# Kernel tuning notes

Measured on AMD Instinct MI355X. Metric: run time of the kernel, lower is better.

The kernel has to match this reference:

```python
import jax, jax.numpy as jnp
import numpy as np

VOCAB = 50000
EMB = 512
HID = 1024
B = 256
W = 26


def setup_inputs() -> dict:
    key = jax.random.key(0)
    k0, k1, k2, k3, k4, k5, k6 = jax.random.split(key, 7)
    s = 1.0 / np.sqrt(HID)
    return {
        "ques_vec": jax.random.randint(k0, (B, W), 0, VOCAB + 1, dtype=jnp.int32),
        "ques_len": jax.random.randint(k1, (B,), 1, W + 1, dtype=jnp.int32),
        # nn.Linear(vocab, emb, bias=False).weight -> [emb, vocab]
        "W_emb": jax.random.normal(k2, (EMB, VOCAB), dtype=jnp.float32) * 0.02,
        # PyTorch LSTM params, gate order (i, f, g, o)
        "W_ih": jax.random.uniform(k3, (4 * HID, EMB), jnp.float32, -s, s),
        "W_hh": jax.random.uniform(k4, (4 * HID, HID), jnp.float32, -s, s),
        "b_ih": jax.random.uniform(k5, (4 * HID,), jnp.float32, -s, s),
        "b_hh": jax.random.uniform(k6, (4 * HID,), jnp.float32, -s, s),
    }


def reference(ques_vec, ques_len, W_emb, W_ih, W_hh, b_ih, b_hh):
    # one_hot(vocab+1)[:, :, 1:] @ W_emb.T  ==  gather of W_emb columns;
    # token 0 (pad) maps to the zero embedding.
    tok = ques_vec  # [B, W]
    emb = jnp.where(
        (tok > 0)[..., None],
        W_emb.T[jnp.maximum(tok - 1, 0)],  # [B, W, EMB]
        jnp.zeros((), dtype=W_emb.dtype),
    )
    emb = jnp.tanh(emb)  # tanh(0)=0 for pads, matches torch

    bias = b_ih + b_hh

    def step(carry, xt):
        h, c = carry
        gates = xt @ W_ih.T + h @ W_hh.T + bias  # [B, 4H]
        i, f, g, o = jnp.split(gates, 4, axis=-1)
        c = jax.nn.sigmoid(f) * c + jax.nn.sigmoid(i) * jnp.tanh(g)
        h = jax.nn.sigmoid(o) * jnpp_tanh(c) if False else jax.nn.sigmoid(o) * jnp.tanh(c)
        return (h, c), None

    h0 = jnp.zeros((tok.shape[0], HID), dtype=W_emb.dtype)
    (h_n, _), _ = jax.lax.scan(step, (h0, h0), jnp.swapaxes(emb, 0, 1))
    return h_n  # [B, HID] == h_n.view(B, -1) for 1-layer unidirectional LSTM
```

## Files before the change

### kernel.cpp

```cpp
#include <hip/hip_runtime.h>
#include <hip/hip_bf16.h>

#define VOCAB 50000
#define EMBD  512
#define HID   1024
#define NB    256
#define SEQW  26
#define MTOT  (SEQW * NB)
#define NGATE (4 * HID)

typedef short short8 __attribute__((ext_vector_type(8)));
typedef _Float16 half8 __attribute__((ext_vector_type(8)));
typedef _Float16 half2v __attribute__((ext_vector_type(2)));
typedef float f32x4  __attribute__((ext_vector_type(4)));
typedef float f32x2  __attribute__((ext_vector_type(2)));

__device__ __forceinline__ unsigned short f16bits(_Float16 h) {
    union { _Float16 h; unsigned short u; } cv; cv.h = h; return cv.u;
}

__device__ __forceinline__ void gload16(const void* g, void* l) {
    __builtin_amdgcn_global_load_lds(
        (const __attribute__((address_space(1))) void*)g,
        (__attribute__((address_space(3))) void*)l, 16, 0, 0);
}

__global__ void init_kernel(unsigned short* __restrict__ hBuf,
                            unsigned int* __restrict__ bar) {
    int idx = blockIdx.x * blockDim.x + threadIdx.x;
    hBuf[idx] = 0;
    if (idx < 4096) bar[idx] = 0;
}

__global__ void transp_kernel(const float* __restrict__ W,
                              unsigned short* __restrict__ WT) {
    __shared__ _Float16 tile[64][72];
    int v0 = blockIdx.x * 64;
    int e0 = blockIdx.y * 64;
    int tid = threadIdx.x;

    int e_loc = tid >> 2, q = tid & 3;
    int vq = q * 16;
    if (v0 + vq < VOCAB) {
        const float* src = W + (size_t)(e0 + e_loc) * VOCAB + v0 + vq;
        #pragma unroll
        for (int j = 0; j < 4; ++j) {
            f32x4 x = *(const f32x4*)(src + 4 * j);
            #pragma unroll
            for (int i = 0; i < 4; ++i)
                tile[vq + 4 * j + i][e_loc] = (_Float16)x[i];
        }
    }
    __syncthreads();

    int v_loc = tid >> 2;
    int ec = q * 16;
    int v = v0 + v_loc;
    if (v < VOCAB) {
        short8* dst = (short8*)(WT + (size_t)v * EMBD + e0 + ec);
        dst[0] = *(const short8*)&tile[v_loc][ec];
        dst[1] = *(const short8*)&tile[v_loc][ec + 8];
    }
}

__global__ void embed_kernel(const int* __restrict__ qv,
                             const unsigned short* __restrict__ WT,
                             unsigned short* __restrict__ eHi) {
    int pair = blockIdx.x * 4 + (threadIdx.x >> 6);
    int t = pair >> 8, b = pair & 255;
    int lane = threadIdx.x & 63;
    int tok = qv[b * SEQW + t];
    short8 out = {};
    if (tok > 0) {
        short8 v = *(const short8*)(WT + (size_t)(tok - 1) * EMBD + lane * 8);
        #pragma unroll
        for (int i = 0; i < 8; ++i) {
            union { short s; _Float16 h; } cv; cv.s = v[i];
            out[i] = (short)f16bits((_Float16)tanhf((float)cv.h));
        }
    }
    *(short8*)(eHi + (size_t)pair * EMBD + lane * 8) = out;
}

__global__ void convw_kernel(const float* __restrict__ Wih,
                             const float* __restrict__ Whh,
                             const float* __restrict__ b_ih,
                             const float* __restrict__ b_hh,
                             unsigned short* __restrict__ ih,
                             unsigned short* __restrict__ hh,
                             float* __restrict__ bsum) {
    int j = blockIdx.x;
    if (threadIdx.x == 0) bsum[j] = b_ih[j] + b_hh[j];
    for (int col = threadIdx.x; col < EMBD; col += blockDim.x)
        ih[(size_t)j * EMBD + col] = f16bits((_Float16)Wih[(size_t)j * EMBD + col]);
    for (int col = threadIdx.x; col < HID; col += blockDim.x)
        hh[(size_t)j * HID + col] = f16bits((_Float16)Whh[(size_t)j * HID + col]);
}

__global__ __launch_bounds__(512, 2) void pregemm_kernel(
    const unsigned short* __restrict__ eHi,
    const unsigned short* __restrict__ ih,
    const float* __restrict__ bsum,
    unsigned short* __restrict__ G0h)
{
    __shared__ char smem[65536];

    int id = blockIdx.x;
    int xcd = id & 7, lid = id >> 3;
    int pc = xcd * 4 + (lid & 3);
    int pm = lid >> 2;
    int m0 = pm * 128;

    int tid = threadIdx.x;
    int w = tid >> 6;
    int mh = w >> 2, nh = w & 3;
    int lane = tid & 63;
    int col16 = lane & 15, g4 = lane >> 4;

    int sr = lane >> 3, sc = lane & 7;
    int ra0 = w * 16 + sr, ra1 = ra0 + 8;
    const char* eB = (const char*)eHi;
    const char* iB = (const char*)ih;
    size_t aOffG0 = (size_t)(m0 + ra0) * 1024 + (size_t)(((sc ^ (ra0 & 7))) * 16);
    size_t aOffG1 = (size_t)(m0 + ra1) * 1024 + (size_t)(((sc ^ (ra1 & 7))) * 16);
    int gb0 = (ra0 >> 5) * 1024 + pc * 32 + (ra0 & 31);
    int gb1 = (ra1 >> 5) * 1024 + pc * 32 + (ra1 & 31);
    size_t bOffG0 = (size_t)gb0 * 1024 + (size_t)(((sc ^ (ra0 & 7))) * 16);
    size_t bOffG1 = (size_t)gb1 * 1024 + (size_t)(((sc ^ (ra1 & 7))) * 16);
    int ldsRow0 = (w * 16) * 128;
    int ldsRow1 = (w * 16 + 8) * 128;

    f32x4 acc[4][2];
    #pragma unroll
    for (int fm = 0; fm < 4; ++fm)
        #pragma unroll
        for (int fn = 0; fn < 2; ++fn)
            acc[fm][fn] = (f32x4){0.f, 0.f, 0.f, 0.f};

    int swb = col16 & 7;
    int aRow[4], bRow[2];
    #pragma unroll
    for (int fm = 0; fm < 4; ++fm) aRow[fm] = (mh * 64 + fm * 16 + col16) * 128;
    #pragma unroll
    for (int fn = 0; fn < 2; ++fn) bRow[fn] = (nh * 32 + fn * 16 + col16) * 128;

#define STAGE(kb, buf) do { \
        int kby = (kb) * 128; \
        char* aD = smem + (buf) * 16384; \
        char* bD = smem + 32768 + (buf) * 16384; \
        gload16(eB + aOffG0 + kby, aD + ldsRow0); \
        gload16(eB + aOffG1 + kby, aD + ldsRow1); \
        gload16(iB + bOffG0 + kby, bD + ldsRow0); \
        gload16(iB + bOffG1 + kby, bD + ldsRow1); \
    } while (0)

    STAGE(0, 0);
    #pragma unroll
    for (int kb = 0; kb < 8; ++kb) {
        int cur = kb & 1;
        __syncthreads();
        if (kb < 7) STAGE(kb + 1, cur ^ 1);
        const char* aS = smem + cur * 16384;
        const char* bS = smem + 32768 + cur * 16384;
        #pragma unroll
        for (int kk = 0; kk < 2; ++kk) {
            int co = ((kk * 4 + g4) ^ swb) * 16;
            half8 bF[2];
            #pragma unroll
            for (int fn = 0; fn < 2; ++fn)
                bF[fn] = *(const half8*)(const void*)(bS + bRow[fn] + co);
            #pragma unroll
            for (int fm = 0; fm < 4; ++fm) {
                half8 aF = *(const half8*)(const void*)(aS + aRow[fm] + co);
                #pragma unroll
                for (int fn = 0; fn < 2; ++fn)
                    acc[fm][fn] = __builtin_amdgcn_mfma_f32_16x16x32_f16(
                        aF, bF[fn], acc[fm][fn], 0, 0, 0);
            }
        }
    }
#undef STAGE

    #pragma unroll
    for (int fn = 0; fn < 2; ++fn) {
        int cp = nh * 32 + fn * 16 + col16;
        int gate = cp >> 5;
        int jh = pc * 32 + (cp & 31);
        int ct = jh >> 4, jl = jh & 15;
        int cidx = gate * 16 + jl;
        float bv = bsum[gate * HID + jh];
        #pragma unroll
        for (int fm = 0; fm < 4; ++fm)
            #pragma unroll
            for (int r = 0; r < 4; ++r) {
                int row = m0 + mh * 64 + fm * 16 + g4 * 4 + r;
                int t = row >> 8, b = row & 255;
                G0h[(((size_t)t * 64 + ct) * 256 + b) * 64 + cidx] =
                    f16bits((_Float16)(acc[fm][fn][r] + bv));
            }
    }
}

__global__ __launch_bounds__(512, 2) void lstm_persist(
    const unsigned short* __restrict__ hh,
    unsigned short* __restrict__ hBuf,
    const unsigned short* __restrict__ G0h,
    float* __restrict__ out,
    unsigned int* __restrict__ bar)
{
    extern __shared__ char smem[];
    float* gbuf = (float*)(smem + 65536);

    int bx = blockIdx.x;
    int grp = bx & 7;
    int lid = bx >> 3;
    int m0  = grp * 32;
    int jh0 = lid * 32;

    int tid = threadIdx.x;
    int w = tid >> 6;
    int kq = w >> 2, gate = w & 3;
    int lane = tid & 63;
    int col16 = lane & 15, g4 = lane >> 4;

    unsigned int* flags = bar + grp * 512;

    half8 bB[2][16];
    #pragma unroll
    for (int nf = 0; nf < 2; ++nf) {
        const char* bRow = (const char*)hh +
            (((size_t)(gate * HID + jh0 + nf * 16 + col16)) * HID + kq * 512 + g4 * 8) * 2;
        #pragma unroll
        for (int kk = 0; kk < 16; ++kk)
            bB[nf][kk] = *(const half8*)(const void*)(bRow + kk * 64);
    }

    int srow = tid >> 4, sc = tid & 15;
    int swz = (srow & 7) << 4;
    int swr = (col16 & 7) << 4;
    int ml = srow, jl2 = sc * 2;
    int jh = jh0 + jl2;
    int ctE = jh >> 4, jlE = jh & 15;

    float cReg[2] = {0.f, 0.f};

    for (int t = 0; t < SEQW; ++t) {
        const unsigned short* hIn = hBuf + (size_t)t * NB * HID;
        unsigned short* hOut = hBuf + (size_t)(t + 1) * NB * HID;

        f32x2 g0v[4];
        {
            const unsigned short* pg = G0h +
                (((size_t)t * 64 + ctE) * 256 + (m0 + ml)) * 64 + jlE;
            #pragma unroll
            for (int q = 0; q < 4; ++q) {
                half2v hv = *(const half2v*)(const void*)(pg + q * 16);
                g0v[q] = (f32x2){(float)hv[0], (float)hv[1]};
            }
        }

        f32x4 acc[2][2];
        #pragma unroll
        for (int mf = 0; mf < 2; ++mf)
            #pragma unroll
            for (int nf = 0; nf < 2; ++nf)
                acc[mf][nf] = (f32x4){0.f, 0.f, 0.f, 0.f};

        if (t > 0) {
            {
                const char* hRowB = (const char*)hIn + (size_t)(m0 + srow) * (HID * 2);
                short8 v[8];
                #pragma unroll
                for (int j = 0; j < 8; ++j)
                    v[j] = *(const short8*)(const void*)(hRowB + j * 256 + sc * 16);
                #pragma unroll
                for (int j = 0; j < 8; ++j)
                    *(short8*)(smem + srow * 2048 + ((j * 256 + sc * 16) ^ swz)) = v[j];
            }
            __syncthreads();

            #pragma unroll
            for (int kk = 0; kk < 16; ++kk) {
                int kb = kq * 1024 + kk * 64 + g4 * 16;
                half8 a0 = *(const half8*)(const void*)(smem + col16 * 2048 + (kb ^ swr));
                half8 a1 = *(const half8*)(const void*)(smem + (col16 + 16) * 2048 + (kb ^ swr));
                acc[0][0] = __builtin_amdgcn_mfma_f32_16x16x32_f16(a0, bB[0][kk], acc[0][0], 0, 0, 0);
                acc[0][1] = __builtin_amdgcn_mfma_f32_16x16x32_f16(a0, bB[1][kk], acc[0][1], 0, 0, 0);
                acc[1][0] = __builtin_amdgcn_mfma_f32_16x16x32_f16(a1, bB[0][kk], acc[1][0], 0, 0, 0);
                acc[1][1] = __builtin_amdgcn_mfma_f32_16x16x32_f16(a1, bB[1][kk], acc[1][1], 0, 0, 0);
            }
        }

        #pragma unroll
        for (int mf = 0; mf < 2; ++mf)
            #pragma unroll
            for (int nf = 0; nf < 2; ++nf)
                #pragma unroll
                for (int r = 0; r < 4; ++r)
                    gbuf[(((kq * 4 + gate) * 32) + mf * 16 + g4 * 4 + r) * 36
                         + nf * 16 + col16] = acc[mf][nf][r];
        __syncthreads();

        f32x2 gv[4];
        #pragma unroll
        for (int q = 0; q < 4; ++q) {
            f32x2 p0 = *(const f32x2*)&gbuf[((q) * 32 + ml) * 36 + jl2];
            f32x2 p1 = *(const f32x2*)&gbuf[((4 + q) * 32 + ml) * 36 + jl2];
            gv[q] = p0 + p1;
        }

        float hN[2];
        #pragma unroll
        for (int u = 0; u < 2; ++u) {
            float gi  = gv[0][u] + g0v[0][u];
            float gf  = gv[1][u] + g0v[1][u];
            float gg_ = gv[2][u] + g0v[2][u];
            float go  = gv[3][u] + g0v[3][u];
            float si = 1.0f / (1.0f + expf(-gi));
            float sf = 1.0f / (1.0f + expf(-gf));
            float so = 1.0f / (1.0f + expf(-go));
            float tg = tanhf(gg_);
            float cN = sf * cReg[u] + si * tg;
            hN[u] = so * tanhf(cN);
            cReg[u] = cN;
        }
        size_t p = (size_t)(m0 + ml) * HID + jh;
        if (t == SEQW - 1) {
            *(f32x2*)(out + p) = (f32x2){hN[0], hN[1]};
        } else {
            unsigned int hv = (unsigned int)f16bits((_Float16)hN[0]) |
                              ((unsigned int)f16bits((_Float16)hN[1]) << 16);
            __hip_atomic_store((unsigned int*)(hOut + p), hv,
                               __ATOMIC_RELAXED, __HIP_MEMORY_SCOPE_AGENT);

            __syncthreads();
            unsigned int t1 = (unsigned int)(t + 1);
            if (tid == 0)
                __hip_atomic_store(flags + lid * 16, t1,
                                   __ATOMIC_RELAXED, __HIP_MEMORY_SCOPE_AGENT);
            if (w == 0) {
                for (;;) {
                    unsigned int v = __hip_atomic_load(
                        flags + (lane & 31) * 16, __ATOMIC_RELAXED,
                        __HIP_MEMORY_SCOPE_AGENT);
                    if (__all(v >= t1)) break;
                    __builtin_amdgcn_s_sleep(1);
                }
            }
            __syncthreads();
        }
    }
}

extern "C" void kernel_launch(void* const* d_in, const int* in_sizes, int n_in,
                              void* d_out, int out_size, void* d_ws, size_t ws_size,
                              hipStream_t stream) {
    const int*   qv   = (const int*)d_in[0];
    const float* Wemb = (const float*)d_in[2];
    const float* Wih  = (const float*)d_in[3];
    const float* Whh  = (const float*)d_in[4];
    const float* b_ih = (const float*)d_in[5];
    const float* b_hh = (const float*)d_in[6];
    float* out = (float*)d_out;

    char* ws = (char*)d_ws;
    size_t off = 0;
    unsigned short* eHi  = (unsigned short*)(ws + off); off += (size_t)MTOT * EMBD * 2;
    unsigned short* ih   = (unsigned short*)(ws + off); off += (size_t)NGATE * EMBD * 2;
    unsigned short* hh   = (unsigned short*)(ws + off); off += (size_t)NGATE * HID * 2;
    unsigned short* hBuf = (unsigned short*)(ws + off); off += (size_t)(SEQW + 1) * NB * HID * 2;
    float* bsum          = (float*)(ws + off);          off += (size_t)NGATE * 4;
    unsigned int* bar    = (unsigned int*)(ws + off);   off += 16384;
    off = (off + 255) & ~(size_t)255;
    unsigned short* G0h  = (unsigned short*)(ws + off); off += (size_t)MTOT * NGATE * 2;
    unsigned short* WembT = (unsigned short*)G0h;

    init_kernel<<<NB * HID / 256, 256, 0, stream>>>(hBuf, bar);
    transp_kernel<<<dim3(782, 8), 256, 0, stream>>>(Wemb, WembT);
    embed_kernel<<<MTOT / 4, 256, 0, stream>>>(qv, WembT, eHi);
    convw_kernel<<<NGATE, 256, 0, stream>>>(Wih, Whh, b_ih, b_hh, ih, hh, bsum);
    pregemm_kernel<<<1664, 512, 0, stream>>>(eHi, ih, bsum, G0h);

    lstm_persist<<<256, 512, 102400, stream>>>(hh, hBuf, G0h, out, bar);
}
```

Measured before the change: 206.7 us.

## Fuse prep kernels, regroup LSTM warp split, interleave gate preactivations

Merges the init, transpose and weight-conversion kernels into one launch, cutting per-launch overhead. Inside the persistent LSTM kernel, warps now split K four ways and each covers all four gates for 64 columns. The gbuf reduction buffer reuses the h-tile shared memory, guarded by an extra barrier, which shrinks dynamic LDS. The precomputed input-gate buffer is reordered so each thread fetches its four gates with one 16-byte load. Barrier flags are packed into one cache line instead of padded slots, which makes polling cheaper but may cause contention on that line.

```diff
diff --git a/kernel.cpp b/kernel.cpp
--- a/kernel.cpp
+++ b/kernel.cpp
@@ -9,9 +9,12 @@
 #define MTOT  (SEQW * NB)
 #define NGATE (4 * HID)
 
+#define TRB 6256
+#define CVB 4096
+#define INB 1024
+
 typedef short short8 __attribute__((ext_vector_type(8)));
 typedef _Float16 half8 __attribute__((ext_vector_type(8)));
-typedef _Float16 half2v __attribute__((ext_vector_type(2)));
 typedef float f32x4  __attribute__((ext_vector_type(4)));
 typedef float f32x2  __attribute__((ext_vector_type(2)));
 
@@ -25,41 +28,55 @@
         (__attribute__((address_space(3))) void*)l, 16, 0, 0);
 }
 
-__global__ void init_kernel(unsigned short* __restrict__ hBuf,
-                            unsigned int* __restrict__ bar) {
-    int idx = blockIdx.x * blockDim.x + threadIdx.x;
-    hBuf[idx] = 0;
-    if (idx < 4096) bar[idx] = 0;
-}
-
-__global__ void transp_kernel(const float* __restrict__ W,
-                              unsigned short* __restrict__ WT) {
-    __shared__ _Float16 tile[64][72];
-    int v0 = blockIdx.x * 64;
-    int e0 = blockIdx.y * 64;
+__global__ void pre_kernel(const float* __restrict__ W,
+                           unsigned short* __restrict__ WT,
+                           const float* __restrict__ Wih,
+                           const float* __restrict__ Whh,
+                           const float* __restrict__ b_ih,
+                           const float* __restrict__ b_hh,
+                           unsigned short* __restrict__ ih,
+                           unsigned short* __restrict__ hh,
+                           float* __restrict__ bsum,
+                           unsigned short* __restrict__ hBuf,
+                           unsigned int* __restrict__ bar) {
+    int bx = blockIdx.x;
     int tid = threadIdx.x;
-
-    int e_loc = tid >> 2, q = tid & 3;
-    int vq = q * 16;
-    if (v0 + vq < VOCAB) {
-        const float* src = W + (size_t)(e0 + e_loc) * VOCAB + v0 + vq;
-        #pragma unroll
-        for (int j = 0; j < 4; ++j) {
-            f32x4 x = *(const f32x4*)(src + 4 * j);
-            #pragma unroll
-            for (int i = 0; i < 4; ++i)
-                tile[vq + 4 * j + i][e_loc] = (_Float16)x[i];
-        }
-    }
-    __syncthreads();
-
-    int v_loc = tid >> 2;
-    int ec = q * 16;
-    int v = v0 + v_loc;
-    if (v < VOCAB) {
-        short8* dst = (short8*)(WT + (size_t)v * EMBD + e0 + ec);
-        dst[0] = *(const short8*)&tile[v_loc][ec];
-        dst[1] = *(const short8*)&tile[v_loc][ec + 8];
+    if (bx < TRB) {
+        __shared__ _Float16 tile[64][72];
+        int v0 = (bx % 782) * 64;
+        int e0 = (bx / 782) * 64;
+        int e_loc = tid >> 2, q = tid & 3;
+        int vq = q * 16;
+        if (v0 + vq < VOCAB) {
+            const float* src = W + (size_t)(e0 + e_loc) * VOCAB + v0 + vq;
+            #pragma unroll
+            for (int j = 0; j < 4; ++j) {
+                f32x4 x = *(const f32x4*)(src + 4 * j);
+                #pragma unroll
+                for (int i = 0; i < 4; ++i)
+                    tile[vq + 4 * j + i][e_loc] = (_Float16)x[i];
+            }
+        }
+        __syncthreads();
+        int v_loc = tid >> 2;
+        int ec = q * 16;
+        int v = v0 + v_loc;
+        if (v < VOCAB) {
+            short8* dst = (short8*)(WT + (size_t)v * EMBD + e0 + ec);
+            dst[0] = *(const short8*)&tile[v_loc][ec];
+            dst[1] = *(const short8*)&tile[v_loc][ec + 8];
+        }
+    } else if (bx < TRB + CVB) {
+        int j = bx - TRB;
+        if (tid == 0) bsum[j] = b_ih[j] + b_hh[j];
+        for (int col = tid; col < EMBD; col += blockDim.x)
+            ih[(size_t)j * EMBD + col] = f16bits((_Float16)Wih[(size_t)j * EMBD + col]);
+        for (int col = tid; col < HID; col += blockDim.x)
+            hh[(size_t)j * HID + col] = f16bits((_Float16)Whh[(size_t)j * HID + col]);
+    } else {
+        int idx = (bx - TRB - CVB) * 256 + tid;
+        hBuf[idx] = 0;
+        if (idx < 4096) bar[idx] = 0;
     }
 }
 
@@ -80,21 +97,6 @@
         }
     }
     *(short8*)(eHi + (size_t)pair * EMBD + lane * 8) = out;
-}
-
-__global__ void convw_kernel(const float* __restrict__ Wih,
-                             const float* __restrict__ Whh,
-                             const float* __restrict__ b_ih,
-                             const float* __restrict__ b_hh,
-                             unsigned short* __restrict__ ih,
-                             unsigned short* __restrict__ hh,
-                             float* __restrict__ bsum) {
-    int j = blockIdx.x;
-    if (threadIdx.x == 0) bsum[j] = b_ih[j] + b_hh[j];
-    for (int col = threadIdx.x; col < EMBD; col += blockDim.x)
-        ih[(size_t)j * EMBD + col] = f16bits((_Float16)Wih[(size_t)j * EMBD + col]);
-    for (int col = threadIdx.x; col < HID; col += blockDim.x)
-        hh[(size_t)j * HID + col] = f16bits((_Float16)Whh[(size_t)j * HID + col]);
 }
 
 __global__ __launch_bounds__(512, 2) void pregemm_kernel(
@@ -187,7 +189,7 @@
         int gate = cp >> 5;
         int jh = pc * 32 + (cp & 31);
         int ct = jh >> 4, jl = jh & 15;
-        int cidx = gate * 16 + jl;
+        int cidx = jl * 4 + gate;
         float bv = bsum[gate * HID + jh];
         #pragma unroll
         for (int fm = 0; fm < 4; ++fm)
@@ -209,7 +211,7 @@
     unsigned int* __restrict__ bar)
 {
     extern __shared__ char smem[];
-    float* gbuf = (float*)(smem + 65536);
+    float* gbuf = (float*)smem;
 
     int bx = blockIdx.x;
     int grp = bx & 7;
@@ -219,19 +221,21 @@
 
     int tid = threadIdx.x;
     int w = tid >> 6;
-    int kq = w >> 2, gate = w & 3;
+    int kq = w & 3, ch = w >> 2;
     int lane = tid & 63;
     int col16 = lane & 15, g4 = lane >> 4;
 
-    unsigned int* flags = bar + grp * 512;
-
-    half8 bB[2][16];
-    #pragma unroll
-    for (int nf = 0; nf < 2; ++nf) {
+    unsigned int* flags = bar + grp * 32;
+
+    half8 bB[4][8];
+    #pragma unroll
+    for (int nf = 0; nf < 4; ++nf) {
+        int colp = ch * 64 + nf * 16 + col16;
+        int gate = colp >> 5, c32 = colp & 31;
         const char* bRow = (const char*)hh +
-            (((size_t)(gate * HID + jh0 + nf * 16 + col16)) * HID + kq * 512 + g4 * 8) * 2;
-        #pragma unroll
-        for (int kk = 0; kk < 16; ++kk)
+            ((size_t)(gate * HID + jh0 + c32) * HID + kq * 256 + g4 * 8) * 2;
+        #pragma unroll
+        for (int kk = 0; kk < 8; ++kk)
             bB[nf][kk] = *(const half8*)(const void*)(bRow + kk * 64);
     }
 
@@ -248,22 +252,18 @@
         const unsigned short* hIn = hBuf + (size_t)t * NB * HID;
         unsigned short* hOut = hBuf + (size_t)(t + 1) * NB * HID;
 
-        f32x2 g0v[4];
+        half8 g0;
         {
             const unsigned short* pg = G0h +
-                (((size_t)t * 64 + ctE) * 256 + (m0 + ml)) * 64 + jlE;
-            #pragma unroll
-            for (int q = 0; q < 4; ++q) {
-                half2v hv = *(const half2v*)(const void*)(pg + q * 16);
-                g0v[q] = (f32x2){(float)hv[0], (float)hv[1]};
-            }
-        }
-
-        f32x4 acc[2][2];
+                (((size_t)t * 64 + ctE) * 256 + (m0 + ml)) * 64 + jlE * 4;
+            g0 = *(const half8*)(const void*)pg;
+        }
+
+        f32x4 acc[2][4];
         #pragma unroll
         for (int mf = 0; mf < 2; ++mf)
             #pragma unroll
-            for (int nf = 0; nf < 2; ++nf)
+            for (int nf = 0; nf < 4; ++nf)
                 acc[mf][nf] = (f32x4){0.f, 0.f, 0.f, 0.f};
 
         if (t > 0) {
@@ -280,46 +280,49 @@
             __syncthreads();
 
             #pragma unroll
-            for (int kk = 0; kk < 16; ++kk) {
-                int kb = kq * 1024 + kk * 64 + g4 * 16;
-                half8 a0 = *(const half8*)(const void*)(smem + col16 * 2048 + (kb ^ swr));
-                half8 a1 = *(const half8*)(const void*)(smem + (col16 + 16) * 2048 + (kb ^ swr));
-                acc[0][0] = __builtin_amdgcn_mfma_f32_16x16x32_f16(a0, bB[0][kk], acc[0][0], 0, 0, 0);
-                acc[0][1] = __builtin_amdgcn_mfma_f32_16x16x32_f16(a0, bB[1][kk], acc[0][1], 0, 0, 0);
-                acc[1][0] = __builtin_amdgcn_mfma_f32_16x16x32_f16(a1, bB[0][kk], acc[1][0], 0, 0, 0);
-                acc[1][1] = __builtin_amdgcn_mfma_f32_16x16x32_f16(a1, bB[1][kk], acc[1][1], 0, 0, 0);
-            }
-        }
+            for (int kk = 0; kk < 8; ++kk) {
+                int kb = kq * 512 + kk * 64 + g4 * 16;
+                int kbs = kb ^ swr;
+                half8 a0 = *(const half8*)(const void*)(smem + col16 * 2048 + kbs);
+                half8 a1 = *(const half8*)(const void*)(smem + (col16 + 16) * 2048 + kbs);
+                #pragma unroll
+                for (int nf = 0; nf < 4; ++nf) {
+                    acc[0][nf] = __builtin_amdgcn_mfma_f32_16x16x32_f16(a0, bB[nf][kk], acc[0][nf], 0, 0, 0);
+                    acc[1][nf] = __builtin_amdgcn_mfma_f32_16x16x32_f16(a1, bB[nf][kk], acc[1][nf], 0, 0, 0);
+                }
+            }
+        }
+        __syncthreads();
 
         #pragma unroll
         for (int mf = 0; mf < 2; ++mf)
             #pragma unroll
-            for (int nf = 0; nf < 2; ++nf)
+            for (int nf = 0; nf < 4; ++nf) {
+                int colp = ch * 64 + nf * 16 + col16;
                 #pragma unroll
                 for (int r = 0; r < 4; ++r)
-                    gbuf[(((kq * 4 + gate) * 32) + mf * 16 + g4 * 4 + r) * 36
-                         + nf * 16 + col16] = acc[mf][nf][r];
+                    gbuf[(kq * 32 + mf * 16 + g4 * 4 + r) * 132 + colp] = acc[mf][nf][r];
+            }
         __syncthreads();
 
-        f32x2 gv[4];
-        #pragma unroll
-        for (int q = 0; q < 4; ++q) {
-            f32x2 p0 = *(const f32x2*)&gbuf[((q) * 32 + ml) * 36 + jl2];
-            f32x2 p1 = *(const f32x2*)&gbuf[((4 + q) * 32 + ml) * 36 + jl2];
-            gv[q] = p0 + p1;
+        float gv[4][2];
+        #pragma unroll
+        for (int g = 0; g < 4; ++g) {
+            f32x2 s = {0.f, 0.f};
+            #pragma unroll
+            for (int q = 0; q < 4; ++q)
+                s += *(const f32x2*)&gbuf[(q * 32 + ml) * 132 + g * 32 + jl2];
+            gv[g][0] = s[0] + (float)g0[g];
+            gv[g][1] = s[1] + (float)g0[4 + g];
         }
 
         float hN[2];
         #pragma unroll
         for (int u = 0; u < 2; ++u) {
-            float gi  = gv[0][u] + g0v[0][u];
-            float gf  = gv[1][u] + g0v[1][u];
-            float gg_ = gv[2][u] + g0v[2][u];
-            float go  = gv[3][u] + g0v[3][u];
-            float si = 1.0f / (1.0f + expf(-gi));
-            float sf = 1.0f / (1.0f + expf(-gf));
-            float so = 1.0f / (1.0f + expf(-go));
-            float tg = tanhf(gg_);
+            float si = 1.0f / (1.0f + expf(-gv[0][u]));
+            float sf = 1.0f / (1.0f + expf(-gv[1][u]));
+            float tg = tanhf(gv[2][u]);
+            float so = 1.0f / (1.0f + expf(-gv[3][u]));
             float cN = sf * cReg[u] + si * tg;
             hN[u] = so * tanhf(cN);
             cReg[u] = cN;
@@ -336,12 +339,12 @@
             __syncthreads();
             unsigned int t1 = (unsigned int)(t + 1);
             if (tid == 0)
-                __hip_atomic_store(flags + lid * 16, t1,
+                __hip_atomic_store(flags + lid, t1,
                                    __ATOMIC_RELAXED, __HIP_MEMORY_SCOPE_AGENT);
             if (w == 0) {
                 for (;;) {
                     unsigned int v = __hip_atomic_load(
-                        flags + (lane & 31) * 16, __ATOMIC_RELAXED,
+                        flags + (lane & 31), __ATOMIC_RELAXED,
                         __HIP_MEMORY_SCOPE_AGENT);
                     if (__all(v >= t1)) break;
                     __builtin_amdgcn_s_sleep(1);
@@ -375,11 +378,10 @@
     unsigned short* G0h  = (unsigned short*)(ws + off); off += (size_t)MTOT * NGATE * 2;
     unsigned short* WembT = (unsigned short*)G0h;
 
-    init_kernel<<<NB * HID / 256, 256, 0, stream>>>(hBuf, bar);
-    transp_kernel<<<dim3(782, 8), 256, 0, stream>>>(Wemb, WembT);
+    pre_kernel<<<TRB + CVB + INB, 256, 0, stream>>>(
+        Wemb, WembT, Wih, Whh, b_ih, b_hh, ih, hh, bsum, hBuf, bar);
     embed_kernel<<<MTOT / 4, 256, 0, stream>>>(qv, WembT, eHi);
-    convw_kernel<<<NGATE, 256, 0, stream>>>(Wih, Whh, b_ih, b_hh, ih, hh, bsum);
     pregemm_kernel<<<1664, 512, 0, stream>>>(eHi, ih, bsum, G0h);
 
-    lstm_persist<<<256, 512, 102400, stream>>>(hh, hBuf, G0h, out, bar);
-}
+    lstm_persist<<<256, 512, 67584, stream>>>(hh, hBuf, G0h, out, bar);
+}
```

Measured after the change: 202.7 us. No clear change (-1.9%).
